# Performance work log

Measured on AMD Instinct MI355X. Metric: run time of the kernel, lower is better.

Reference implementation:

```python
import jax, jax.numpy as jnp
import numpy as np

EPS = 1e-13


def masked_softmax(vector, mask, axis):
    # Faithful to the original (memory_efficient=False path):
    # softmax(vector * mask), re-mask, renormalize.
    m = mask.astype(vector.dtype)
    result = jax.nn.softmax(vector * m, axis=axis) * m
    return result / (result.sum(axis=axis, keepdims=True) + EPS)


def setup_inputs() -> dict:
    key = jax.random.key(0)
    ks = jax.random.split(key, 9)
    B, L1, L2, D, A = 32, 1024, 1024, 256, 128
    inp = {
        "seq_features1": jax.random.normal(ks[0], (B, L1, D), dtype=jnp.float32),
        "seq_features2": jax.random.normal(ks[1], (B, L2, D), dtype=jnp.float32),
        "mask1": jax.random.randint(ks[2], (B, L1), 0, 2, dtype=jnp.int32),
        "mask2": jax.random.randint(ks[3], (B, L2), 0, 2, dtype=jnp.int32),
        # xavier-ish scaling to keep tanh out of saturation
        "W": jax.random.normal(ks[4], (D, D), dtype=jnp.float32) * (1.0 / np.sqrt(D)),
        "Wv": jax.random.normal(ks[5], (D, A), dtype=jnp.float32) * (1.0 / np.sqrt(D)),
        "Wq": jax.random.normal(ks[6], (D, A), dtype=jnp.float32) * (1.0 / np.sqrt(D)),
        "w_hv": jax.random.normal(ks[7], (A, 1), dtype=jnp.float32) * (1.0 / np.sqrt(A)),
        "w_hq": jax.random.normal(ks[8], (A, 1), dtype=jnp.float32) * (1.0 / np.sqrt(A)),
    }
    return inp


def reference(seq_features1, seq_features2, mask1, mask2, W, Wv, Wq, w_hv, w_hq):
    f1, f2 = seq_features1, seq_features2
    # C: [B, L1, L2] affinity matrix  (tanh(f1 W f2^T))
    C = jnp.tanh(jnp.einsum("bld,dm->blm", f1, W) @ jnp.swapaxes(f2, 1, 2))
    f1Wv = f1 @ Wv                      # [B, L1, A]
    f2Wq = f2 @ Wq                      # [B, L2, A]
    Hv = jnp.tanh(f1Wv + C @ f2Wq)      # [B, L1, A]
    Hq = jnp.tanh(f2Wq + jnp.swapaxes(C, 1, 2) @ f1Wv)  # [B, L2, A]
    attn_v = masked_softmax((Hv @ w_hv)[..., 0], mask1, axis=1)  # [B, L1]
    attn_q = masked_softmax((Hq @ w_hq)[..., 0], mask2, axis=1)  # [B, L2]
    v_hat = jnp.sum(attn_v[..., None] * f1, axis=1)  # [B, D]
    q_hat = jnp.sum(attn_q[..., None] * f2, axis=1)  # [B, D]
    return (v_hat, q_hat)
```

## Files before the change

### kernel.cpp

```cpp
#include <hip/hip_runtime.h>
#include <math.h>

#define L_SEQ 1024
#define DDIM  256
#define ADIM  128
#define NB    32

typedef __attribute__((ext_vector_type(8))) short bf16x8;
typedef __attribute__((ext_vector_type(4))) float f32x4;
typedef __attribute__((ext_vector_type(16))) float f32x16;

__device__ __forceinline__ ushort f2bf(float x) {
    uint u = __builtin_bit_cast(uint, x);
    u = (u + 0x7FFFu + ((u >> 16) & 1u)) >> 16;
    return (ushort)u;
}
__device__ __forceinline__ float bf2f(ushort h) {
    uint u = ((uint)h) << 16;
    return __builtin_bit_cast(float, u);
}
__device__ __forceinline__ float tanh_fast(float x) {
    float ax = fabsf(x);
    float e  = __expf(ax * -2.0f);
    float r  = (1.0f - e) * __builtin_amdgcn_rcpf(1.0f + e);
    return copysignf(r, x);
}
__device__ __forceinline__ uint cvtpk_bf16(float lo, float hi) {
    uint r;
    asm("v_cvt_pk_bf16_f32 %0, %1, %2" : "=v"(r) : "v"(lo), "v"(hi));
    return r;
}
__device__ __forceinline__ void async_copy16(ushort* lds_dst, const ushort* g_src) {
    __builtin_amdgcn_global_load_lds(
        (const __attribute__((address_space(1))) unsigned int*)(g_src),
        (__attribute__((address_space(3))) unsigned int*)(lds_dst),
        16, 0, 0);
}
__device__ __forceinline__ void async_copy16f(float* lds_dst, const float* g_src) {
    __builtin_amdgcn_global_load_lds(
        (const __attribute__((address_space(1))) unsigned int*)(g_src),
        (__attribute__((address_space(3))) unsigned int*)(lds_dst),
        16, 0, 0);
}

__global__ __launch_bounds__(256) void cvt_bf16(const float* __restrict__ in,
                                                ushort* __restrict__ out, int n) {
    int i = (blockIdx.x * 256 + threadIdx.x) * 8;
    if (i >= n) return;
    float4 a = *reinterpret_cast<const float4*>(&in[i]);
    float4 b = *reinterpret_cast<const float4*>(&in[i + 4]);
    ushort4 lo = { f2bf(a.x), f2bf(a.y), f2bf(a.z), f2bf(a.w) };
    ushort4 hi = { f2bf(b.x), f2bf(b.y), f2bf(b.z), f2bf(b.w) };
    *reinterpret_cast<ushort4*>(&out[i]) = lo;
    *reinterpret_cast<ushort4*>(&out[i + 4]) = hi;
}

__global__ __launch_bounds__(512) void wt_prep_all(
        const float* __restrict__ W,  const float* __restrict__ Wv,
        const float* __restrict__ Wq,
        ushort* __restrict__ WTh, ushort* __restrict__ WvTh,
        ushort* __restrict__ WqTh) {
    int k = blockIdx.x;
    int t = threadIdx.x;
    const float* src; ushort* dh; int n, nn;
    if (t < 256)      { src = W;  dh = WTh;  n = t;       nn = 256; }
    else if (t < 384) { src = Wv; dh = WvTh; n = t - 256; nn = 128; }
    else              { src = Wq; dh = WqTh; n = t - 384; nn = 128; }
    ushort* dl = dh + (size_t)nn * 256;
    float x = src[(size_t)k * nn + n];
    ushort hh = f2bf(x);
    dh[(size_t)n * 256 + k] = hh;
    dl[(size_t)n * 256 + k] = f2bf(x - bf2f(hh));
}

__global__ __launch_bounds__(256, 2) void proj2_mfma(
        const float* __restrict__ A, const ushort* __restrict__ BTh,
        ushort* __restrict__ C, int N) {
    __shared__ float  As[128 * 64];
    __shared__ ushort Bs[128 * 128];

    const int tid  = threadIdx.x;
    const int lane = tid & 63;
    const int wid  = tid >> 6;
    const int l31  = lane & 31;
    const int h    = lane >> 5;
    const int m0   = blockIdx.y * 128;
    const int n0   = blockIdx.x * 128;
    const int wrow = wid * 32;
    const int row  = wrow + l31;
    const int rsw  = row & 15;

    int aoff[8], boff[8];
    #pragma unroll
    for (int it = 0; it < 8; ++it) {
        int idx = it * 256 + tid;
        int r   = idx >> 4, g = idx & 15;
        int gx  = g ^ (r & 15);
        aoff[it] = (m0 + r) * 256 + gx * 4;
        int gxB  = g ^ (r & 15);
        boff[it] = (n0 + r) * 256 + (gxB & 7) * 8 + ((gxB & 8) ? N * 256 : 0);
    }

    f32x16 acc[4];
    #pragma unroll
    for (int i = 0; i < 4; ++i)
        #pragma unroll
        for (int j = 0; j < 16; ++j) acc[i][j] = 0.f;

    for (int kc = 0; kc < 4; ++kc) {
        const int k0 = kc * 64;
        __syncthreads();
        #pragma unroll
        for (int it = 0; it < 8; ++it) {
            async_copy16f(&As[it * 1024 + wid * 256], A + aoff[it] + k0);
            async_copy16(&Bs[it * 2048 + wid * 512], BTh + boff[it] + k0);
        }
        __syncthreads();

        #pragma unroll
        for (int s = 0; s < 4; ++s) {
            int ga = s * 4 + h * 2;
            float4 alo = *reinterpret_cast<const float4*>(&As[(row * 16 + (ga ^ rsw)) * 4]);
            float4 ahi = *reinterpret_cast<const float4*>(&As[(row * 16 + ((ga + 1) ^ rsw)) * 4]);
            uint ah0 = cvtpk_bf16(alo.x, alo.y);
            uint ah1 = cvtpk_bf16(alo.z, alo.w);
            uint ah2 = cvtpk_bf16(ahi.x, ahi.y);
            uint ah3 = cvtpk_bf16(ahi.z, ahi.w);
            float r0 = alo.x - __builtin_bit_cast(float, ah0 << 16);
            float r1 = alo.y - __builtin_bit_cast(float, ah0 & 0xffff0000u);
            float r2 = alo.z - __builtin_bit_cast(float, ah1 << 16);
            float r3 = alo.w - __builtin_bit_cast(float, ah1 & 0xffff0000u);
            float r4 = ahi.x - __builtin_bit_cast(float, ah2 << 16);
            float r5 = ahi.y - __builtin_bit_cast(float, ah2 & 0xffff0000u);
            float r6 = ahi.z - __builtin_bit_cast(float, ah3 << 16);
            float r7 = ahi.w - __builtin_bit_cast(float, ah3 & 0xffff0000u);
            uint al0 = cvtpk_bf16(r0, r1), al1 = cvtpk_bf16(r2, r3);
            uint al2 = cvtpk_bf16(r4, r5), al3 = cvtpk_bf16(r6, r7);
            union { uint u[4]; bf16x8 v; } uh = {{ah0, ah1, ah2, ah3}};
            union { uint u[4]; bf16x8 v; } ul = {{al0, al1, al2, al3}};
            bf16x8 ah = uh.v, al = ul.v;

            #pragma unroll
            for (int nf = 0; nf < 4; ++nf) {
                int col = nf * 32 + l31;
                int csw = col & 15;
                int gb  = s * 2 + h;
                bf16x8 bh = *reinterpret_cast<const bf16x8*>(&Bs[col * 128 + (gb ^ csw) * 8]);
                bf16x8 bl = *reinterpret_cast<const bf16x8*>(&Bs[col * 128 + ((gb + 8) ^ csw) * 8]);
                acc[nf] = __builtin_amdgcn_mfma_f32_32x32x16_bf16(ah, bh, acc[nf], 0, 0, 0);
                acc[nf] = __builtin_amdgcn_mfma_f32_32x32x16_bf16(ah, bl, acc[nf], 0, 0, 0);
                acc[nf] = __builtin_amdgcn_mfma_f32_32x32x16_bf16(al, bh, acc[nf], 0, 0, 0);
            }
        }
    }

    #pragma unroll
    for (int nf = 0; nf < 4; ++nf)
        #pragma unroll
        for (int reg = 0; reg < 16; ++reg) {
            int rowl = (reg & 3) + 8 * (reg >> 2) + 4 * h;
            C[(size_t)(m0 + wrow + rowl) * N + n0 + nf * 32 + l31] = f2bf(acc[nf][reg]);
        }
}

__global__ __launch_bounds__(256, 2) void fused_logits_mfma(
        const ushort* __restrict__ f1Wb, const ushort* __restrict__ f2b,
        const ushort* __restrict__ f1Wvb, const ushort* __restrict__ f2Wqb,
        const float* __restrict__ w_hv,  const float* __restrict__ w_hq,
        float* __restrict__ lo_v, float* __restrict__ lo_q) {
    __shared__ ushort KsU[2 * 32 * 256];
    __shared__ ushort VtU[2 * 128 * 40];

    const int tid  = threadIdx.x;
    const int lane = tid & 63;
    const int wid  = tid >> 6;
    const int l31  = lane & 31;
    const int h    = lane >> 5;
    const int h8   = h * 8;
    const int kxor = (l31 & 15) << 3;

    const int wg   = blockIdx.x;
    const int xcd  = wg & 7;
    const int t    = wg >> 3;
    const int b    = xcd * 4 + (t >> 4);
    const int rem  = t & 15;
    const int z    = rem >> 3;
    const int r0   = (rem & 7) * 128;

    const ushort* Qb = z ? f2b   : f1Wb;
    const ushort* Kb = z ? f1Wb  : f2b;
    const ushort* Vg = z ? f1Wvb : f2Wqb;
    const ushort* Bg = z ? f2Wqb : f1Wvb;
    const float*  w  = z ? w_hq  : w_hv;
    float* logits    = z ? lo_q  : lo_v;

    const int qrow = r0 + wid * 32 + l31;
    const ushort* qp = Qb + ((size_t)b * L_SEQ + qrow) * DDIM + h8;
    bf16x8 qf[16];
    #pragma unroll
    for (int st = 0; st < 16; ++st)
        qf[st] = *reinterpret_cast<const bf16x8*>(&qp[st * 16]);

    int koff[4];
    #pragma unroll
    for (int it = 0; it < 4; ++it) {
        int rr  = wid * 8 + it * 2 + h;
        int col = (8 * l31) ^ ((rr & 15) << 3);
        koff[it] = rr * 256 + col;
    }
    const int va0 = tid & 127,          vk0 = tid >> 7;
    const int va1 = (tid + 256) & 127,  vk1 = (tid + 256) >> 7;

    f32x16 acc[4];
    #pragma unroll
    for (int i = 0; i < 4; ++i)
        #pragma unroll
        for (int j = 0; j < 16; ++j) acc[i][j] = 0.f;

    uint4 vr0, vr1;

    {
        const ushort* gK = Kb + (size_t)b * L_SEQ * DDIM;
        #pragma unroll
        for (int it = 0; it < 4; ++it)
            async_copy16(&KsU[(wid * 8 + it * 2) * 256], gK + koff[it]);
        const ushort* gV = Vg + (size_t)b * L_SEQ * ADIM;
        union { uint4 v4; ushort us[8]; } u;
        const ushort* s0 = gV + (size_t)vk0 * 8 * ADIM + va0;
        #pragma unroll
        for (int j = 0; j < 8; ++j) u.us[j] = s0[(size_t)j * ADIM];
        vr0 = u.v4;
        const ushort* s1 = gV + (size_t)vk1 * 8 * ADIM + va1;
        #pragma unroll
        for (int j = 0; j < 8; ++j) u.us[j] = s1[(size_t)j * ADIM];
        vr1 = u.v4;
        *reinterpret_cast<uint4*>(&VtU[va0 * 40 + vk0 * 8]) = vr0;
        *reinterpret_cast<uint4*>(&VtU[va1 * 40 + vk1 * 8]) = vr1;
    }
    __syncthreads();

    int cur = 0;
    for (int c0 = 0; c0 < L_SEQ; c0 += 32) {
        const int nxt = cur ^ 1;
        const ushort* Kc = &KsU[cur * (32 * 256)];
        const ushort* Vc = &VtU[cur * (128 * 40)];
        const bool more = (c0 + 32 < L_SEQ);

        if (more) {
            ushort* Kn = &KsU[nxt * (32 * 256)];
            const ushort* gK = Kb + ((size_t)b * L_SEQ + c0 + 32) * DDIM;
            #pragma unroll
            for (int it = 0; it < 4; ++it)
                async_copy16(&Kn[(wid * 8 + it * 2) * 256], gK + koff[it]);
            const ushort* gV = Vg + ((size_t)b * L_SEQ + c0 + 32) * ADIM;
            union { uint4 v4; ushort us[8]; } u;
            const ushort* s0 = gV + (size_t)vk0 * 8 * ADIM + va0;
            #pragma unroll
            for (int j = 0; j < 8; ++j) u.us[j] = s0[(size_t)j * ADIM];
            vr0 = u.v4;
            const ushort* s1 = gV + (size_t)vk1 * 8 * ADIM + va1;
            #pragma unroll
            for (int j = 0; j < 8; ++j) u.us[j] = s1[(size_t)j * ADIM];
            vr1 = u.v4;
        }

        f32x16 sA, sB;
        #pragma unroll
        for (int j = 0; j < 16; ++j) { sA[j] = 0.f; sB[j] = 0.f; }
        #pragma unroll
        for (int st = 0; st < 8; ++st) {
            bf16x8 k0 = *reinterpret_cast<const bf16x8*>(
                &Kc[l31 * 256 + (((2 * st) * 16 + h8) ^ kxor)]);
            bf16x8 k1 = *reinterpret_cast<const bf16x8*>(
                &Kc[l31 * 256 + (((2 * st + 1) * 16 + h8) ^ kxor)]);
            sA = __builtin_amdgcn_mfma_f32_32x32x16_bf16(k0, qf[2 * st],     sA, 0, 0, 0);
            sB = __builtin_amdgcn_mfma_f32_32x32x16_bf16(k1, qf[2 * st + 1], sB, 0, 0, 0);
        }
        uint c0p = cvtpk_bf16(tanh_fast(sA[0]  + sB[0]),  tanh_fast(sA[1]  + sB[1]));
        uint c1p = cvtpk_bf16(tanh_fast(sA[2]  + sB[2]),  tanh_fast(sA[3]  + sB[3]));
        uint c2p = cvtpk_bf16(tanh_fast(sA[4]  + sB[4]),  tanh_fast(sA[5]  + sB[5]));
        uint c3p = cvtpk_bf16(tanh_fast(sA[6]  + sB[6]),  tanh_fast(sA[7]  + sB[7]));
        uint c4p = cvtpk_bf16(tanh_fast(sA[8]  + sB[8]),  tanh_fast(sA[9]  + sB[9]));
        uint c5p = cvtpk_bf16(tanh_fast(sA[10] + sB[10]), tanh_fast(sA[11] + sB[11]));
        uint c6p = cvtpk_bf16(tanh_fast(sA[12] + sB[12]), tanh_fast(sA[13] + sB[13]));
        uint c7p = cvtpk_bf16(tanh_fast(sA[14] + sB[14]), tanh_fast(sA[15] + sB[15]));
        asm("v_permlane32_swap_b32 %0, %1" : "+v"(c0p), "+v"(c2p));
        asm("v_permlane32_swap_b32 %0, %1" : "+v"(c1p), "+v"(c3p));
        asm("v_permlane32_swap_b32 %0, %1" : "+v"(c4p), "+v"(c6p));
        asm("v_permlane32_swap_b32 %0, %1" : "+v"(c5p), "+v"(c7p));
        union { uint u[4]; bf16x8 v; } pu0 = {{c0p, c1p, c2p, c3p}};
        union { uint u[4]; bf16x8 v; } pu1 = {{c4p, c5p, c6p, c7p}};
        bf16x8 pa0 = pu0.v, pa1 = pu1.v;

        #pragma unroll
        for (int nt = 0; nt < 4; ++nt) {
            bf16x8 vb0 = *reinterpret_cast<const bf16x8*>(&Vc[(nt * 32 + l31) * 40 + h8]);
            acc[nt] = __builtin_amdgcn_mfma_f32_32x32x16_bf16(pa0, vb0, acc[nt], 0, 0, 0);
        }
        #pragma unroll
        for (int nt = 0; nt < 4; ++nt) {
            bf16x8 vb1 = *reinterpret_cast<const bf16x8*>(&Vc[(nt * 32 + l31) * 40 + 16 + h8]);
            acc[nt] = __builtin_amdgcn_mfma_f32_32x32x16_bf16(pa1, vb1, acc[nt], 0, 0, 0);
        }

        if (more) {
            ushort* Vn = &VtU[nxt * (128 * 40)];
            *reinterpret_cast<uint4*>(&Vn[va0 * 40 + vk0 * 8]) = vr0;
            *reinterpret_cast<uint4*>(&Vn[va1 * 40 + vk1 * 8]) = vr1;
        }
        __syncthreads();
        cur = nxt;
    }

    float wv[4];
    #pragma unroll
    for (int nt = 0; nt < 4; ++nt) wv[nt] = w[nt * 32 + l31];
    const size_t bbase = ((size_t)b * L_SEQ + r0) * ADIM;
    #pragma unroll
    for (int reg = 0; reg < 16; ++reg) {
        int rowl = (reg & 3) + 8 * (reg >> 2) + 4 * h;
        int row  = wid * 32 + rowl;
        float p = 0.f;
        #pragma unroll
        for (int nt = 0; nt < 4; ++nt) {
            float bias = bf2f(Bg[bbase + (size_t)row * ADIM + nt * 32 + l31]);
            p = fmaf(tanh_fast(bias + acc[nt][reg]), wv[nt], p);
        }
        p += __shfl_xor(p, 1);
        p += __shfl_xor(p, 2);
        p += __shfl_xor(p, 4);
        p += __shfl_xor(p, 8);
        p += __shfl_xor(p, 16);
        if (l31 == 0) logits[(size_t)b * L_SEQ + r0 + row] = p;
    }
}

__global__ __launch_bounds__(256) void attn_softmax(
        const float* __restrict__ lo_v, const float* __restrict__ lo_q,
        const int* __restrict__ mask1,  const int* __restrict__ mask2,
        float* __restrict__ att) {
    __shared__ float red[256];
    const int tid = threadIdx.x;
    const int b   = blockIdx.x;
    const int sel = blockIdx.y;
    const float* logits = sel ? lo_q : lo_v;
    const int*   mask   = sel ? mask2 : mask1;
    float* ao = att + ((size_t)sel * NB + b) * L_SEQ;

    float z[4], m[4];
    float lmax = -1e30f;
    #pragma unroll
    for (int i = 0; i < 4; ++i) {
        int l = i * 256 + tid;
        float lv = logits[(size_t)b * L_SEQ + l];
        m[i] = (float)mask[(size_t)b * L_SEQ + l];
        z[i] = lv * m[i];
        lmax = fmaxf(lmax, z[i]);
    }
    red[tid] = lmax; __syncthreads();
    for (int s = 128; s > 0; s >>= 1) {
        if (tid < s) red[tid] = fmaxf(red[tid], red[tid + s]);
        __syncthreads();
    }
    const float mx = red[0];
    __syncthreads();

    float p[4], lsum = 0.f;
    #pragma unroll
    for (int i = 0; i < 4; ++i) { p[i] = expf(z[i] - mx); lsum += p[i]; }
    red[tid] = lsum; __syncthreads();
    for (int s = 128; s > 0; s >>= 1) {
        if (tid < s) red[tid] += red[tid + s];
        __syncthreads();
    }
    const float Z = red[0];
    __syncthreads();

    float r[4], rsum = 0.f;
    #pragma unroll
    for (int i = 0; i < 4; ++i) { r[i] = (p[i] / Z) * m[i]; rsum += r[i]; }
    red[tid] = rsum; __syncthreads();
    for (int s = 128; s > 0; s >>= 1) {
        if (tid < s) red[tid] += red[tid + s];
        __syncthreads();
    }
    const float denom = red[0] + 1e-13f;

    #pragma unroll
    for (int i = 0; i < 4; ++i) ao[i * 256 + tid] = r[i] / denom;
}

__global__ __launch_bounds__(256) void wsum_partial(
        const float* __restrict__ att, const float* __restrict__ f1,
        const float* __restrict__ f2,  float* __restrict__ partial) {
    __shared__ float a_s[128];
    const int tid = threadIdx.x;
    const int b   = blockIdx.x;
    const int sel = blockIdx.y;
    const int z   = blockIdx.z;
    const int l0  = z * 128;
    const float* ap = att + ((size_t)sel * NB + b) * L_SEQ + l0;
    if (tid < 128) a_s[tid] = ap[tid];
    __syncthreads();
    const float* f = sel ? f2 : f1;
    const float* fb = f + ((size_t)b * L_SEQ + l0) * DDIM + tid;
    float acc = 0.f;
    #pragma unroll 4
    for (int j = 0; j < 128; ++j)
        acc = fmaf(a_s[j], fb[(size_t)j * DDIM], acc);
    partial[(((size_t)z * 2 + sel) * NB + b) * DDIM + tid] = acc;
}

__global__ __launch_bounds__(256) void wsum_reduce(
        const float* __restrict__ partial, float* __restrict__ out) {
    const int tid = threadIdx.x;
    const int sb  = blockIdx.x;
    float s = 0.f;
    #pragma unroll
    for (int zz = 0; zz < 8; ++zz)
        s += partial[((size_t)zz * 64 + sb) * DDIM + tid];
    out[(size_t)sb * DDIM + tid] = s;
}

extern "C" void kernel_launch(void* const* d_in, const int* in_sizes, int n_in,
                              void* d_out, int out_size, void* d_ws, size_t ws_size,
                              hipStream_t stream) {
    const float* f1    = (const float*)d_in[0];
    const float* f2    = (const float*)d_in[1];
    const int*   mask1 = (const int*)d_in[2];
    const int*   mask2 = (const int*)d_in[3];
    const float* W     = (const float*)d_in[4];
    const float* Wv    = (const float*)d_in[5];
    const float* Wq    = (const float*)d_in[6];
    const float* w_hv  = (const float*)d_in[7];
    const float* w_hq  = (const float*)d_in[8];
    float* out = (float*)d_out;

    ushort* f2b   = (ushort*)d_ws;
    ushort* f1Wb  = f2b   + 8388608;
    ushort* f1Wvb = f1Wb  + 8388608;
    ushort* f2Wqb = f1Wvb + 4194304;
    ushort* WTh   = f2Wqb + 4194304;
    ushort* WvTh  = WTh   + 131072;
    ushort* WqTh  = WvTh  + 65536;
    float*  lo_v  = (float*)(WqTh + 65536);
    float*  lo_q  = lo_v + 32768;
    float*  att   = lo_q + 32768;
    float*  part  = att  + 65536;

    wt_prep_all<<<256, 512, 0, stream>>>(W, Wv, Wq, WTh, WvTh, WqTh);
    cvt_bf16<<<4096, 256, 0, stream>>>(f2, f2b, 8388608);

    proj2_mfma<<<dim3(2, 256), 256, 0, stream>>>(f1, WTh,  f1Wb,  256);
    proj2_mfma<<<dim3(1, 256), 256, 0, stream>>>(f1, WvTh, f1Wvb, 128);
    proj2_mfma<<<dim3(1, 256), 256, 0, stream>>>(f2, WqTh, f2Wqb, 128);

    fused_logits_mfma<<<512, 256, 0, stream>>>(
        f1Wb, f2b, f1Wvb, f2Wqb, w_hv, w_hq, lo_v, lo_q);

    attn_softmax<<<dim3(NB, 2), 256, 0, stream>>>(lo_v, lo_q, mask1, mask2, att);
    wsum_partial<<<dim3(NB, 2, 8), 256, 0, stream>>>(att, f1, f2, part);
    wsum_reduce<<<64, 256, 0, stream>>>(part, out);
}
```

Measured before the change: 162.5 us.

## Merge prep and projection launches, software-pipeline PV MFMAs, fuse softmax into weighted sum

Weight transposition and f2 bf16 conversion now run in one kernel, and the three projection GEMMs run in one launch dispatched by block index. In the fused logits kernel, the P·V MFMAs for the previous chunk are delayed one iteration and issued next to the current QK MFMAs. The V LDS buffer becomes triple-buffered for this, and setprio raises wave priority around the MFMA block. Softmax is recomputed per z-slice inside the weighted-sum kernel, which removes the att round trip and one launch at the cost of redundant softmax work across 8 blocks.

```diff
diff --git a/kernel.cpp b/kernel.cpp
--- a/kernel.cpp
+++ b/kernel.cpp
@@ -43,49 +43,58 @@
         16, 0, 0);
 }
 
-__global__ __launch_bounds__(256) void cvt_bf16(const float* __restrict__ in,
-                                                ushort* __restrict__ out, int n) {
-    int i = (blockIdx.x * 256 + threadIdx.x) * 8;
-    if (i >= n) return;
-    float4 a = *reinterpret_cast<const float4*>(&in[i]);
-    float4 b = *reinterpret_cast<const float4*>(&in[i + 4]);
-    ushort4 lo = { f2bf(a.x), f2bf(a.y), f2bf(a.z), f2bf(a.w) };
-    ushort4 hi = { f2bf(b.x), f2bf(b.y), f2bf(b.z), f2bf(b.w) };
-    *reinterpret_cast<ushort4*>(&out[i]) = lo;
-    *reinterpret_cast<ushort4*>(&out[i + 4]) = hi;
-}
-
-__global__ __launch_bounds__(512) void wt_prep_all(
+__global__ __launch_bounds__(256) void wt_cvt(
         const float* __restrict__ W,  const float* __restrict__ Wv,
-        const float* __restrict__ Wq,
+        const float* __restrict__ Wq, const float* __restrict__ f2,
         ushort* __restrict__ WTh, ushort* __restrict__ WvTh,
-        ushort* __restrict__ WqTh) {
-    int k = blockIdx.x;
-    int t = threadIdx.x;
-    const float* src; ushort* dh; int n, nn;
-    if (t < 256)      { src = W;  dh = WTh;  n = t;       nn = 256; }
-    else if (t < 384) { src = Wv; dh = WvTh; n = t - 256; nn = 128; }
-    else              { src = Wq; dh = WqTh; n = t - 384; nn = 128; }
-    ushort* dl = dh + (size_t)nn * 256;
-    float x = src[(size_t)k * nn + n];
-    ushort hh = f2bf(x);
-    dh[(size_t)n * 256 + k] = hh;
-    dl[(size_t)n * 256 + k] = f2bf(x - bf2f(hh));
-}
-
-__global__ __launch_bounds__(256, 2) void proj2_mfma(
-        const float* __restrict__ A, const ushort* __restrict__ BTh,
-        ushort* __restrict__ C, int N) {
+        ushort* __restrict__ WqTh, ushort* __restrict__ f2b) {
+    const int bid = blockIdx.x;
+    const int tid = threadIdx.x;
+    if (bid < 256) {
+        int k = bid;
+        #pragma unroll
+        for (int t = tid; t < 512; t += 256) {
+            const float* src; ushort* dh; int n, nn;
+            if (t < 256)      { src = W;  dh = WTh;  n = t;       nn = 256; }
+            else if (t < 384) { src = Wv; dh = WvTh; n = t - 256; nn = 128; }
+            else              { src = Wq; dh = WqTh; n = t - 384; nn = 128; }
+            ushort* dl = dh + (size_t)nn * 256;
+            float x = src[(size_t)k * nn + n];
+            ushort hh = f2bf(x);
+            dh[(size_t)n * 256 + k] = hh;
+            dl[(size_t)n * 256 + k] = f2bf(x - bf2f(hh));
+        }
+    } else {
+        int i = ((bid - 256) * 256 + tid) * 8;
+        float4 a = *reinterpret_cast<const float4*>(&f2[i]);
+        float4 b = *reinterpret_cast<const float4*>(&f2[i + 4]);
+        ushort4 lo = { f2bf(a.x), f2bf(a.y), f2bf(a.z), f2bf(a.w) };
+        ushort4 hi = { f2bf(b.x), f2bf(b.y), f2bf(b.z), f2bf(b.w) };
+        *reinterpret_cast<ushort4*>(&f2b[i]) = lo;
+        *reinterpret_cast<ushort4*>(&f2b[i + 4]) = hi;
+    }
+}
+
+__global__ __launch_bounds__(256, 2) void proj_all(
+        const float* __restrict__ f1, const float* __restrict__ f2,
+        const ushort* __restrict__ WTh, const ushort* __restrict__ WvTh,
+        const ushort* __restrict__ WqTh,
+        ushort* __restrict__ f1Wb, ushort* __restrict__ f1Wvb,
+        ushort* __restrict__ f2Wqb) {
     __shared__ float  As[128 * 64];
     __shared__ ushort Bs[128 * 128];
+
+    const int bid = blockIdx.x;
+    const float* A; const ushort* BTh; ushort* C; int N, m0, n0;
+    if (bid < 512)      { A = f1; BTh = WTh;  C = f1Wb;  N = 256; m0 = (bid >> 1) * 128; n0 = (bid & 1) * 128; }
+    else if (bid < 768) { A = f1; BTh = WvTh; C = f1Wvb; N = 128; m0 = (bid - 512) * 128; n0 = 0; }
+    else                { A = f2; BTh = WqTh; C = f2Wqb; N = 128; m0 = (bid - 768) * 128; n0 = 0; }
 
     const int tid  = threadIdx.x;
     const int lane = tid & 63;
     const int wid  = tid >> 6;
     const int l31  = lane & 31;
     const int h    = lane >> 5;
-    const int m0   = blockIdx.y * 128;
-    const int n0   = blockIdx.x * 128;
     const int wrow = wid * 32;
     const int row  = wrow + l31;
     const int rsw  = row & 15;
@@ -97,8 +106,7 @@
         int r   = idx >> 4, g = idx & 15;
         int gx  = g ^ (r & 15);
         aoff[it] = (m0 + r) * 256 + gx * 4;
-        int gxB  = g ^ (r & 15);
-        boff[it] = (n0 + r) * 256 + (gxB & 7) * 8 + ((gxB & 8) ? N * 256 : 0);
+        boff[it] = (n0 + r) * 256 + (gx & 7) * 8 + ((gx & 8) ? N * 256 : 0);
     }
 
     f32x16 acc[4];
@@ -169,7 +177,7 @@
         const float* __restrict__ w_hv,  const float* __restrict__ w_hq,
         float* __restrict__ lo_v, float* __restrict__ lo_q) {
     __shared__ ushort KsU[2 * 32 * 256];
-    __shared__ ushort VtU[2 * 128 * 40];
+    __shared__ ushort VtU[3 * 128 * 40];
 
     const int tid  = threadIdx.x;
     const int lane = tid & 63;
@@ -218,6 +226,7 @@
         for (int j = 0; j < 16; ++j) acc[i][j] = 0.f;
 
     uint4 vr0, vr1;
+    bf16x8 pa0 = {}, pa1 = {};
 
     {
         const ushort* gK = Kb + (size_t)b * L_SEQ * DDIM;
@@ -239,20 +248,18 @@
     }
     __syncthreads();
 
-    int cur = 0;
-    for (int c0 = 0; c0 < L_SEQ; c0 += 32) {
-        const int nxt = cur ^ 1;
-        const ushort* Kc = &KsU[cur * (32 * 256)];
-        const ushort* Vc = &VtU[cur * (128 * 40)];
-        const bool more = (c0 + 32 < L_SEQ);
+    for (int c = 0; c < 32; ++c) {
+        const int kcur = c & 1;
+        const ushort* Kc = &KsU[kcur * (32 * 256)];
+        const bool more = (c + 1 < 32);
 
         if (more) {
-            ushort* Kn = &KsU[nxt * (32 * 256)];
-            const ushort* gK = Kb + ((size_t)b * L_SEQ + c0 + 32) * DDIM;
+            ushort* Kn = &KsU[(kcur ^ 1) * (32 * 256)];
+            const ushort* gK = Kb + ((size_t)b * L_SEQ + (c + 1) * 32) * DDIM;
             #pragma unroll
             for (int it = 0; it < 4; ++it)
                 async_copy16(&Kn[(wid * 8 + it * 2) * 256], gK + koff[it]);
-            const ushort* gV = Vg + ((size_t)b * L_SEQ + c0 + 32) * ADIM;
+            const ushort* gV = Vg + ((size_t)b * L_SEQ + (c + 1) * 32) * ADIM;
             union { uint4 v4; ushort us[8]; } u;
             const ushort* s0 = gV + (size_t)vk0 * 8 * ADIM + va0;
             #pragma unroll
@@ -267,6 +274,7 @@
         f32x16 sA, sB;
         #pragma unroll
         for (int j = 0; j < 16; ++j) { sA[j] = 0.f; sB[j] = 0.f; }
+        __builtin_amdgcn_s_setprio(1);
         #pragma unroll
         for (int st = 0; st < 8; ++st) {
             bf16x8 k0 = *reinterpret_cast<const bf16x8*>(
@@ -276,6 +284,21 @@
             sA = __builtin_amdgcn_mfma_f32_32x32x16_bf16(k0, qf[2 * st],     sA, 0, 0, 0);
             sB = __builtin_amdgcn_mfma_f32_32x32x16_bf16(k1, qf[2 * st + 1], sB, 0, 0, 0);
         }
+        if (c > 0) {
+            const ushort* Vp = &VtU[((c + 2) % 3) * (128 * 40)];
+            #pragma unroll
+            for (int nt = 0; nt < 4; ++nt) {
+                bf16x8 vb0 = *reinterpret_cast<const bf16x8*>(&Vp[(nt * 32 + l31) * 40 + h8]);
+                acc[nt] = __builtin_amdgcn_mfma_f32_32x32x16_bf16(pa0, vb0, acc[nt], 0, 0, 0);
+            }
+            #pragma unroll
+            for (int nt = 0; nt < 4; ++nt) {
+                bf16x8 vb1 = *reinterpret_cast<const bf16x8*>(&Vp[(nt * 32 + l31) * 40 + 16 + h8]);
+                acc[nt] = __builtin_amdgcn_mfma_f32_32x32x16_bf16(pa1, vb1, acc[nt], 0, 0, 0);
+            }
+        }
+        __builtin_amdgcn_s_setprio(0);
+
         uint c0p = cvtpk_bf16(tanh_fast(sA[0]  + sB[0]),  tanh_fast(sA[1]  + sB[1]));
         uint c1p = cvtpk_bf16(tanh_fast(sA[2]  + sB[2]),  tanh_fast(sA[3]  + sB[3]));
         uint c2p = cvtpk_bf16(tanh_fast(sA[4]  + sB[4]),  tanh_fast(sA[5]  + sB[5]));
@@ -290,26 +313,28 @@
         asm("v_permlane32_swap_b32 %0, %1" : "+v"(c5p), "+v"(c7p));
         union { uint u[4]; bf16x8 v; } pu0 = {{c0p, c1p, c2p, c3p}};
         union { uint u[4]; bf16x8 v; } pu1 = {{c4p, c5p, c6p, c7p}};
-        bf16x8 pa0 = pu0.v, pa1 = pu1.v;
-
-        #pragma unroll
-        for (int nt = 0; nt < 4; ++nt) {
-            bf16x8 vb0 = *reinterpret_cast<const bf16x8*>(&Vc[(nt * 32 + l31) * 40 + h8]);
-            acc[nt] = __builtin_amdgcn_mfma_f32_32x32x16_bf16(pa0, vb0, acc[nt], 0, 0, 0);
-        }
-        #pragma unroll
-        for (int nt = 0; nt < 4; ++nt) {
-            bf16x8 vb1 = *reinterpret_cast<const bf16x8*>(&Vc[(nt * 32 + l31) * 40 + 16 + h8]);
-            acc[nt] = __builtin_amdgcn_mfma_f32_32x32x16_bf16(pa1, vb1, acc[nt], 0, 0, 0);
-        }
+        pa0 = pu0.v; pa1 = pu1.v;
 
         if (more) {
-            ushort* Vn = &VtU[nxt * (128 * 40)];
+            ushort* Vn = &VtU[((c + 1) % 3) * (128 * 40)];
             *reinterpret_cast<uint4*>(&Vn[va0 * 40 + vk0 * 8]) = vr0;
             *reinterpret_cast<uint4*>(&Vn[va1 * 40 + vk1 * 8]) = vr1;
         }
         __syncthreads();
-        cur = nxt;
+    }
+
+    {
+        const ushort* Vp = &VtU[(31 % 3) * (128 * 40)];
+        #pragma unroll
+        for (int nt = 0; nt < 4; ++nt) {
+            bf16x8 vb0 = *reinterpret_cast<const bf16x8*>(&Vp[(nt * 32 + l31) * 40 + h8]);
+            acc[nt] = __builtin_amdgcn_mfma_f32_32x32x16_bf16(pa0, vb0, acc[nt], 0, 0, 0);
+        }
+        #pragma unroll
+        for (int nt = 0; nt < 4; ++nt) {
+            bf16x8 vb1 = *reinterpret_cast<const bf16x8*>(&Vp[(nt * 32 + l31) * 40 + 16 + h8]);
+            acc[nt] = __builtin_amdgcn_mfma_f32_32x32x16_bf16(pa1, vb1, acc[nt], 0, 0, 0);
+        }
     }
 
     float wv[4];
@@ -335,17 +360,19 @@
     }
 }
 
-__global__ __launch_bounds__(256) void attn_softmax(
+__global__ __launch_bounds__(256) void softmax_wsum(
         const float* __restrict__ lo_v, const float* __restrict__ lo_q,
         const int* __restrict__ mask1,  const int* __restrict__ mask2,
-        float* __restrict__ att) {
+        const float* __restrict__ f1,   const float* __restrict__ f2,
+        float* __restrict__ partial) {
+    __shared__ float rs[L_SEQ];
     __shared__ float red[256];
     const int tid = threadIdx.x;
     const int b   = blockIdx.x;
     const int sel = blockIdx.y;
+    const int zz  = blockIdx.z;
     const float* logits = sel ? lo_q : lo_v;
     const int*   mask   = sel ? mask2 : mask1;
-    float* ao = att + ((size_t)sel * NB + b) * L_SEQ;
 
     float z[4], m[4];
     float lmax = -1e30f;
@@ -384,31 +411,21 @@
         if (tid < s) red[tid] += red[tid + s];
         __syncthreads();
     }
-    const float denom = red[0] + 1e-13f;
-
-    #pragma unroll
-    for (int i = 0; i < 4; ++i) ao[i * 256 + tid] = r[i] / denom;
-}
-
-__global__ __launch_bounds__(256) void wsum_partial(
-        const float* __restrict__ att, const float* __restrict__ f1,
-        const float* __restrict__ f2,  float* __restrict__ partial) {
-    __shared__ float a_s[128];
-    const int tid = threadIdx.x;
-    const int b   = blockIdx.x;
-    const int sel = blockIdx.y;
-    const int z   = blockIdx.z;
-    const int l0  = z * 128;
-    const float* ap = att + ((size_t)sel * NB + b) * L_SEQ + l0;
-    if (tid < 128) a_s[tid] = ap[tid];
+    const float inv = 1.0f / (red[0] + 1e-13f);
     __syncthreads();
-    const float* f = sel ? f2 : f1;
+
+    #pragma unroll
+    for (int i = 0; i < 4; ++i) rs[i * 256 + tid] = r[i] * inv;
+    __syncthreads();
+
+    const int l0 = zz * 128;
+    const float* f  = sel ? f2 : f1;
     const float* fb = f + ((size_t)b * L_SEQ + l0) * DDIM + tid;
     float acc = 0.f;
     #pragma unroll 4
     for (int j = 0; j < 128; ++j)
-        acc = fmaf(a_s[j], fb[(size_t)j * DDIM], acc);
-    partial[(((size_t)z * 2 + sel) * NB + b) * DDIM + tid] = acc;
+        acc = fmaf(rs[l0 + j], fb[(size_t)j * DDIM], acc);
+    partial[(((size_t)zz * 2 + sel) * NB + b) * DDIM + tid] = acc;
 }
 
 __global__ __launch_bounds__(256) void wsum_reduce(
@@ -445,20 +462,17 @@
     ushort* WqTh  = WvTh  + 65536;
     float*  lo_v  = (float*)(WqTh + 65536);
     float*  lo_q  = lo_v + 32768;
-    float*  att   = lo_q + 32768;
-    float*  part  = att  + 65536;
-
-    wt_prep_all<<<256, 512, 0, stream>>>(W, Wv, Wq, WTh, WvTh, WqTh);
-    cvt_bf16<<<4096, 256, 0, stream>>>(f2, f2b, 8388608);
-
-    proj2_mfma<<<dim3(2, 256), 256, 0, stream>>>(f1, WTh,  f1Wb,  256);
-    proj2_mfma<<<dim3(1, 256), 256, 0, stream>>>(f1, WvTh, f1Wvb, 128);
-    proj2_mfma<<<dim3(1, 256), 256, 0, stream>>>(f2, WqTh, f2Wqb, 128);
+    float*  part  = lo_q + 32768;
+
+    wt_cvt<<<4352, 256, 0, stream>>>(W, Wv, Wq, f2, WTh, WvTh, WqTh, f2b);
+
+    proj_all<<<1024, 256, 0, stream>>>(f1, f2, WTh, WvTh, WqTh,
+                                       f1Wb, f1Wvb, f2Wqb);
 
     fused_logits_mfma<<<512, 256, 0, stream>>>(
         f1Wb, f2b, f1Wvb, f2Wqb, w_hv, w_hq, lo_v, lo_q);
 
-    attn_softmax<<<dim3(NB, 2), 256, 0, stream>>>(lo_v, lo_q, mask1, mask2, att);
-    wsum_partial<<<dim3(NB, 2, 8), 256, 0, stream>>>(att, f1, f2, part);
+    softmax_wsum<<<dim3(NB, 2, 8), 256, 0, stream>>>(
+        lo_v, lo_q, mask1, mask2, f1, f2, part);
     wsum_reduce<<<64, 256, 0, stream>>>(part, out);
 }
```

Measured after the change: 142.8 us. 12.2% less time.
